# Performance work log

Hardware: AMD Instinct MI355X
Metric: run time of the kernel (lower is better)

## Reference

```python
import jax, jax.numpy as jnp
import numpy as np

N_NODES = 300000   # cell instances
N_NETS  = 200000   # hyperedges (nets); each net has exactly one source/driver
E_SINK  = 1000000  # sink (node->net) pin edges
NODE_DIM, NET_DIM, EMB = 32, 16, 64
L, NUM_VN = 3, 1000
OUT_NODE, OUT_NET = 4, 4
SLOPE = 0.01  # torch leaky_relu default negative_slope


def leaky(x):
    return jnp.where(x >= 0, x, SLOPE * x)


def _lin(key, fan_in, fan_out):
    kw, kb = jax.random.split(key)
    b = 1.0 / np.sqrt(fan_in)
    W = jax.random.uniform(kw, (fan_in, fan_out), jnp.float32, -b, b)
    bb = jax.random.uniform(kb, (fan_out,), jnp.float32, -b, b)
    return W, bb


def setup_inputs() -> dict:
    key = jax.random.key(0)
    ks = iter(jax.random.split(key, 64))
    d = {}
    d["node_features"] = jax.random.normal(next(ks), (N_NODES, NODE_DIM), jnp.float32)
    d["net_features"] = jax.random.normal(next(ks), (N_NETS, NET_DIM), jnp.float32)
    d["src_nodes"] = jax.random.randint(next(ks), (N_NETS,), 0, N_NODES)   # driver node of net i
    d["sink_nodes"] = jax.random.randint(next(ks), (E_SINK,), 0, N_NODES)
    d["sink_nets"] = jax.random.randint(next(ks), (E_SINK,), 0, N_NETS)
    d["edge_weight"] = jax.random.uniform(next(ks), (E_SINK,), jnp.float32)
    d["batch"] = jax.random.randint(next(ks), (N_NODES,), 0, NUM_VN)       # node -> virtual node id
    # node / net encoders
    d["ne_W1"], d["ne_b1"] = _lin(next(ks), NODE_DIM, 2 * EMB)
    d["ne_W2"], d["ne_b2"] = _lin(next(ks), 2 * EMB, EMB)
    d["te_W1"], d["te_b1"] = _lin(next(ks), NET_DIM, EMB)
    d["te_W2"], d["te_b2"] = _lin(next(ks), EMB, EMB)
    d["vn_emb"] = jnp.zeros((EMB,), jnp.float32)  # torch: init.constant_(weight, 0)
    # HyperConv layers, stacked over L
    Wnet, bnet, Wnode, bnode = [], [], [], []
    for _ in range(L):
        W, b = _lin(next(ks), 3 * EMB, EMB); Wnet.append(W); bnet.append(b)
        W, b = _lin(next(ks), 2 * EMB, EMB); Wnode.append(W); bnode.append(b)
    d["conv_Wnet"] = jnp.stack(Wnet); d["conv_bnet"] = jnp.stack(bnet)
    d["conv_Wnode"] = jnp.stack(Wnode); d["conv_bnode"] = jnp.stack(bnode)
    # virtual-node MLPs (L-1 of them)
    vW1, vb1, vW2, vb2 = [], [], [], []
    for _ in range(L - 1):
        W, b = _lin(next(ks), EMB, EMB); vW1.append(W); vb1.append(b)
        W, b = _lin(next(ks), EMB, EMB); vW2.append(W); vb2.append(b)
    d["vn_W1"] = jnp.stack(vW1); d["vn_b1"] = jnp.stack(vb1)
    d["vn_W2"] = jnp.stack(vW2); d["vn_b2"] = jnp.stack(vb2)
    # output heads
    d["fc1n_W"], d["fc1n_b"] = _lin(next(ks), EMB, 256)
    d["fc2n_W"], d["fc2n_b"] = _lin(next(ks), 256, OUT_NODE)
    d["fc1e_W"], d["fc1e_b"] = _lin(next(ks), EMB, 64)
    d["fc2e_W"], d["fc2e_b"] = _lin(next(ks), 64, OUT_NET)
    return d


def _forward(node_features, net_features, edge_weight,
             ne_W1, ne_b1, ne_W2, ne_b2, te_W1, te_b1, te_W2, te_b2,
             vn_emb, conv_Wnet, conv_bnet, conv_Wnode, conv_bnode,
             vn_W1, vn_b1, vn_W2, vn_b2,
             fc1n_W, fc1n_b, fc2n_W, fc2n_b, fc1e_W, fc1e_b, fc2e_W, fc2e_b,
             src_nodes, sink_nodes, sink_nets, batch):
    h = leaky(node_features @ ne_W1 + ne_b1) @ ne_W2 + ne_b2   # [N, EMB]
    g = leaky(net_features @ te_W1 + te_b1) @ te_W2 + te_b2    # [M, EMB]
    w = edge_weight[:, None]
    vn = jnp.broadcast_to(vn_emb, (NUM_VN, EMB))               # embedding of all-zero indices
    for l in range(L):
        h = h + vn[batch]
        # node -> net (hyperedge) aggregation: driver message + weighted sink sum
        agg_src = h[src_nodes]                                             # [M, EMB]
        agg_sink = jax.ops.segment_sum(h[sink_nodes] * w, sink_nets, num_segments=N_NETS)
        g = jnp.concatenate([g, agg_src, agg_sink], axis=-1) @ conv_Wnet[l] + conv_bnet[l]
        # net -> node aggregation
        back = jax.ops.segment_sum(g, src_nodes, num_segments=N_NODES) \
             + jax.ops.segment_sum(g[sink_nets] * w, sink_nodes, num_segments=N_NODES)
        h = jnp.concatenate([h, back], axis=-1) @ conv_Wnode[l] + conv_bnode[l]
        h = leaky(h)
        g = leaky(g)
        if l < L - 1:
            pooled = jax.ops.segment_max(h, batch, num_segments=NUM_VN)   # global_max_pool
            tmp = pooled + vn
            vn = vn + (leaky(tmp @ vn_W1[l] + vn_b1[l]) @ vn_W2[l] + vn_b2[l])
    node_rep = jnp.abs(leaky(h @ fc1n_W + fc1n_b) @ fc2n_W + fc2n_b)
    net_rep = jnp.abs(leaky(g @ fc1e_W + fc1e_b) @ fc2e_W + fc2e_b)
    return node_rep, net_rep


def reference(node_features, net_features, edge_weight,
              ne_W1, ne_b1, ne_W2, ne_b2, te_W1, te_b1, te_W2, te_b2,
              vn_emb, conv_Wnet, conv_bnet, conv_Wnode, conv_bnode,
              vn_W1, vn_b1, vn_W2, vn_b2,
              fc1n_W, fc1n_b, fc2n_W, fc2n_b, fc1e_W, fc1e_b, fc2e_W, fc2e_b,
              src_nodes, sink_nodes, sink_nets, batch):
    return _forward(node_features, net_features, edge_weight,
                    ne_W1, ne_b1, ne_W2, ne_b2, te_W1, te_b1, te_W2, te_b2,
                    vn_emb, conv_Wnet, conv_bnet, conv_Wnode, conv_bnode,
                    vn_W1, vn_b1, vn_W2, vn_b2,
                    fc1n_W, fc1n_b, fc2n_W, fc2n_b, fc1e_W, fc1e_b, fc2e_W, fc2e_b,
                    src_nodes, sink_nodes, sink_nets, batch)
```

## Files before the change

kernel.cpp:

```cpp
#include <hip/hip_runtime.h>
#include <cstdint>

static constexpr int N_NODES = 300000;
static constexpr int N_NETS  = 200000;
static constexpr int E_SINK  = 1000000;
static constexpr int NODE_DIM = 32;
static constexpr int NET_DIM  = 16;
static constexpr int EMB = 64;
static constexpr int NUM_VN = 1000;
#define SLOPE 0.01f

typedef __attribute__((ext_vector_type(8))) short bhalf8;
typedef __attribute__((ext_vector_type(4))) float floatx4;
typedef unsigned short u16;

__device__ __forceinline__ float leaky(float x) { return x >= 0.f ? x : SLOPE * x; }

__device__ __forceinline__ unsigned bf16_rne(float x) {
    unsigned u = __float_as_uint(x);
    return (u + 0x7FFFu + ((u >> 16) & 1u)) >> 16;
}
__device__ __forceinline__ void split1(float x, u16& hh, u16& ll) {
    unsigned hb = bf16_rne(x);
    float fh = __uint_as_float(hb << 16);
    unsigned lb = bf16_rne(x - fh);
    hh = (u16)hb; ll = (u16)lb;
}
__device__ __forceinline__ void split8v(const float* x, bhalf8& ah, bhalf8& al) {
#pragma unroll
    for (int e = 0; e < 8; ++e) {
        u16 hh, ll; split1(x[e], hh, ll);
        ah[e] = (short)hh; al[e] = (short)ll;
    }
}
__device__ __forceinline__ float rec1(short h, short l) {
    return __uint_as_float(((unsigned)(u16)h) << 16) +
           __uint_as_float(((unsigned)(u16)l) << 16);
}

__device__ __forceinline__ void afrag_f32(const float* rowp, int kbase, bhalf8& ah, bhalf8& al) {
    float4 v0 = *(const float4*)(rowp + kbase);
    float4 v1 = *(const float4*)(rowp + kbase + 4);
    float x[8] = {v0.x, v0.y, v0.z, v0.w, v1.x, v1.y, v1.z, v1.w};
    split8v(x, ah, al);
}
__device__ __forceinline__ void afrag_hl(const u16* hi, const u16* lo, size_t off,
                                         bhalf8& ah, bhalf8& al) {
    ah = *(const bhalf8*)(hi + off);
    al = *(const bhalf8*)(lo + off);
}

__device__ __forceinline__ floatx4 mm3(bhalf8 ah, bhalf8 al, bhalf8 wh, bhalf8 wl, floatx4 c) {
    c = __builtin_amdgcn_mfma_f32_16x16x32_bf16(ah, wh, c, 0, 0, 0);
    c = __builtin_amdgcn_mfma_f32_16x16x32_bf16(ah, wl, c, 0, 0, 0);
    c = __builtin_amdgcn_mfma_f32_16x16x32_bf16(al, wh, c, 0, 0, 0);
    return c;
}

static constexpr int OFF_NEW1 = 0;
static constexpr int OFF_NEW2 = 4096;
static constexpr int OFF_TEW1 = 12288;
static constexpr int OFF_TEW2 = 14336;
static constexpr int OFF_CWNET = 18432;
static constexpr int OFF_CWNODE = 55296;
static constexpr int OFF_FC1N = 79872;
static constexpr int OFF_FC1E = 96256;
static constexpr int W_TOTAL  = 100352;

__global__ void k_prep_w(const float* __restrict__ neW1, const float* __restrict__ neW2,
                         const float* __restrict__ teW1, const float* __restrict__ teW2,
                         const float* __restrict__ cWnet, const float* __restrict__ cWnode,
                         const float* __restrict__ fc1n, const float* __restrict__ fc1e,
                         u16* __restrict__ wfh, u16* __restrict__ wfl)
{
    int i = blockIdx.x * 256 + threadIdx.x;
    if (i >= W_TOTAL) return;
    int r, ncols, K; const float* src;
    if (i < OFF_NEW2)        { r = i;             src = neW1;  ncols = 128; K = 32; }
    else if (i < OFF_TEW1)   { r = i - OFF_NEW2;  src = neW2;  ncols = 64;  K = 128; }
    else if (i < OFF_TEW2)   { r = i - OFF_TEW1;  src = teW1;  ncols = 64;  K = 16; }
    else if (i < OFF_CWNET)  { r = i - OFF_TEW2;  src = teW2;  ncols = 64;  K = 64; }
    else if (i < OFF_CWNODE) { int t = i - OFF_CWNET;  int l = t / 12288; r = t % 12288;
                               src = cWnet + (size_t)l * 192 * 64; ncols = 64; K = 192; }
    else if (i < OFF_FC1N)   { int t = i - OFF_CWNODE; int l = t / 8192;  r = t % 8192;
                               src = cWnode + (size_t)l * 128 * 64; ncols = 64; K = 128; }
    else if (i < OFF_FC1E)   { r = i - OFF_FC1N;  src = fc1n;  ncols = 256; K = 64; }
    else                     { r = i - OFF_FC1E;  src = fc1e;  ncols = 64;  K = 64; }
    int e = r & 7, g = (r >> 3) & 3;
    int cidx = r >> 5;
    int col = cidx % ncols, kt = cidx / ncols;
    int k = kt * 32 + g * 8 + e;
    float v = (k < K) ? src[(size_t)k * ncols + col] : 0.f;
    u16 hh, ll; split1(v, hh, ll);
    wfh[i] = hh; wfl[i] = ll;
}

__device__ __forceinline__ bhalf8 ldw(const u16* p, int idx) {
    return *(const bhalf8*)(p + idx);
}

__global__ void k_hist_edges(const int* __restrict__ sink_nets, const int* __restrict__ sink_nodes,
                             int* __restrict__ cnt_net, int* __restrict__ cnt_node)
{
    int e = blockIdx.x * 256 + threadIdx.x;
    if (e >= E_SINK) return;
    atomicAdd(&cnt_net[sink_nets[e]], 1);
    atomicAdd(&cnt_node[sink_nodes[e]], 1);
}

__global__ void k_hist_misc(const int* __restrict__ src_nodes, const int* __restrict__ batch,
                            int* __restrict__ cnt_src, int* __restrict__ cnt_vn)
{
    int i = blockIdx.x * 256 + threadIdx.x;
    if (i < N_NETS) atomicAdd(&cnt_src[src_nodes[i]], 1);
    if (i < N_NODES) atomicAdd(&cnt_vn[batch[i]], 1);
}

__global__ void k_scan1(const int* __restrict__ cnt, int n, int* __restrict__ bsum) {
    __shared__ int s[256];
    int i = blockIdx.x * 256 + threadIdx.x;
    s[threadIdx.x] = (i < n) ? cnt[i] : 0;
    __syncthreads();
    for (int off = 128; off; off >>= 1) {
        if (threadIdx.x < off) s[threadIdx.x] += s[threadIdx.x + off];
        __syncthreads();
    }
    if (threadIdx.x == 0) bsum[blockIdx.x] = s[0];
}

__global__ void k_scan2(int* __restrict__ data, int n) {
    __shared__ int s[256];
    __shared__ int carry_s;
    int tid = threadIdx.x;
    if (tid == 0) carry_s = 0;
    __syncthreads();
    for (int base = 0; base < n; base += 256) {
        int i = base + tid;
        int v = (i < n) ? data[i] : 0;
        s[tid] = v;
        __syncthreads();
        for (int off = 1; off < 256; off <<= 1) {
            int t = (tid >= off) ? s[tid - off] : 0;
            __syncthreads();
            s[tid] += t;
            __syncthreads();
        }
        int excl = s[tid] - v + carry_s;
        if (i < n) data[i] = excl;
        __syncthreads();
        if (tid == 255) carry_s = excl + v;
        __syncthreads();
    }
}

__global__ void k_scan3(const int* __restrict__ cnt, int n, const int* __restrict__ bsum,
                        int* __restrict__ start) {
    __shared__ int s[256];
    int i = blockIdx.x * 256 + threadIdx.x;
    int v = (i < n) ? cnt[i] : 0;
    s[threadIdx.x] = v;
    __syncthreads();
    for (int off = 1; off < 256; off <<= 1) {
        int t = (threadIdx.x >= off) ? s[threadIdx.x - off] : 0;
        __syncthreads();
        s[threadIdx.x] += t;
        __syncthreads();
    }
    int excl = s[threadIdx.x] - v + bsum[blockIdx.x];
    if (i < n) start[i] = excl;
    if (i == n - 1) start[n] = excl + v;
}

__global__ void k_fill_edges(const int* __restrict__ sink_nets, const int* __restrict__ sink_nodes,
                             const float* __restrict__ ew,
                             const int* __restrict__ net_start, const int* __restrict__ node_start,
                             int* __restrict__ cur_net, int* __restrict__ cur_node,
                             int2* __restrict__ e_pack, int2* __restrict__ e2_pack)
{
    int e = blockIdx.x * 256 + threadIdx.x;
    if (e >= E_SINK) return;
    int tn = sink_nets[e], dn = sink_nodes[e];
    int wbits = __float_as_int(ew[e]);
    int p = net_start[tn] + atomicAdd(&cur_net[tn], 1);
    e_pack[p] = make_int2(dn, wbits);
    int q = node_start[dn] + atomicAdd(&cur_node[dn], 1);
    e2_pack[q] = make_int2(tn, wbits);
}

__global__ void k_fill_misc(const int* __restrict__ src_nodes, const int* __restrict__ batch,
                            const int* __restrict__ src_start, const int* __restrict__ vn_start,
                            int* __restrict__ cur_src, int* __restrict__ cur_vn,
                            int* __restrict__ s_net, int* __restrict__ b_node)
{
    int i = blockIdx.x * 256 + threadIdx.x;
    if (i < N_NETS) {
        int d = src_nodes[i];
        int p = src_start[d] + atomicAdd(&cur_src[d], 1);
        s_net[p] = i;
    }
    if (i < N_NODES) {
        int v = batch[i];
        int p = vn_start[v] + atomicAdd(&cur_vn[v], 1);
        b_node[p] = i;
    }
}

template<bool HF32>
__global__ __launch_bounds__(256) void k_gather_agg(
    u16* __restrict__ agg_hi, u16* __restrict__ agg_lo,
    const u16* __restrict__ h_hi, const u16* __restrict__ h_lo, const float* __restrict__ h_f32,
    const int* __restrict__ net_start, const int2* __restrict__ e_pack)
{
    int w = (blockIdx.x * 256 + threadIdx.x) >> 6;
    if (w >= N_NETS) return;
    int lane = threadIdx.x & 63;
    int grp = lane >> 3, l8 = lane & 7;
    int j0 = net_start[w], j1 = net_start[w + 1];
    float a[8] = {0.f, 0.f, 0.f, 0.f, 0.f, 0.f, 0.f, 0.f};
    for (int j = j0 + grp; j < j1; j += 8) {
        int2 pk = e_pack[j];
        float wt = __int_as_float(pk.y);
        if (HF32) {
            const float4* rp = (const float4*)(h_f32 + (size_t)pk.x * 64 + l8 * 8);
            float4 v0 = rp[0], v1 = rp[1];
            a[0] += wt * v0.x; a[1] += wt * v0.y; a[2] += wt * v0.z; a[3] += wt * v0.w;
            a[4] += wt * v1.x; a[5] += wt * v1.y; a[6] += wt * v1.z; a[7] += wt * v1.w;
        } else {
            size_t off = (size_t)pk.x * 64 + l8 * 8;
            bhalf8 vh = *(const bhalf8*)(h_hi + off);
            bhalf8 vl = *(const bhalf8*)(h_lo + off);
#pragma unroll
            for (int e = 0; e < 8; ++e) a[e] += wt * rec1(vh[e], vl[e]);
        }
    }
#pragma unroll
    for (int e = 0; e < 8; ++e) {
        a[e] += __shfl_xor(a[e], 8, 64);
        a[e] += __shfl_xor(a[e], 16, 64);
        a[e] += __shfl_xor(a[e], 32, 64);
    }
    if (grp == 0) {
        bhalf8 oh, ol;
        split8v(a, oh, ol);
        size_t off = (size_t)w * 64 + l8 * 8;
        *(bhalf8*)(agg_hi + off) = oh;
        *(bhalf8*)(agg_lo + off) = ol;
    }
}

template<bool GF32>
__global__ __launch_bounds__(256) void k_gather_back(
    u16* __restrict__ back_hi, u16* __restrict__ back_lo,
    const u16* __restrict__ g_hi, const u16* __restrict__ g_lo, const float* __restrict__ g_raw,
    const int* __restrict__ src_start, const int* __restrict__ s_net,
    const int* __restrict__ node_start, const int2* __restrict__ e2_pack)
{
    int w = (blockIdx.x * 256 + threadIdx.x) >> 6;
    if (w >= N_NODES) return;
    int lane = threadIdx.x & 63;
    int grp = lane >> 3, l8 = lane & 7;
    float a[8] = {0.f, 0.f, 0.f, 0.f, 0.f, 0.f, 0.f, 0.f};
    int j0 = src_start[w], j1 = src_start[w + 1];
    for (int j = j0 + grp; j < j1; j += 8) {
        int idx = s_net[j];
        if (GF32) {
            const float4* rp = (const float4*)(g_raw + (size_t)idx * 64 + l8 * 8);
            float4 v0 = rp[0], v1 = rp[1];
            a[0] += v0.x; a[1] += v0.y; a[2] += v0.z; a[3] += v0.w;
            a[4] += v1.x; a[5] += v1.y; a[6] += v1.z; a[7] += v1.w;
        } else {
            size_t off = (size_t)idx * 64 + l8 * 8;
            bhalf8 vh = *(const bhalf8*)(g_hi + off);
            bhalf8 vl = *(const bhalf8*)(g_lo + off);
#pragma unroll
            for (int e = 0; e < 8; ++e) {
                float f = rec1(vh[e], vl[e]);
                a[e] += (f >= 0.f) ? f : f * 100.f;
            }
        }
    }
    j0 = node_start[w]; j1 = node_start[w + 1];
    for (int j = j0 + grp; j < j1; j += 8) {
        int2 pk = e2_pack[j];
        float wt = __int_as_float(pk.y);
        if (GF32) {
            const float4* rp = (const float4*)(g_raw + (size_t)pk.x * 64 + l8 * 8);
            float4 v0 = rp[0], v1 = rp[1];
            a[0] += wt * v0.x; a[1] += wt * v0.y; a[2] += wt * v0.z; a[3] += wt * v0.w;
            a[4] += wt * v1.x; a[5] += wt * v1.y; a[6] += wt * v1.z; a[7] += wt * v1.w;
        } else {
            size_t off = (size_t)pk.x * 64 + l8 * 8;
            bhalf8 vh = *(const bhalf8*)(g_hi + off);
            bhalf8 vl = *(const bhalf8*)(g_lo + off);
#pragma unroll
            for (int e = 0; e < 8; ++e) {
                float f = rec1(vh[e], vl[e]);
                a[e] += wt * ((f >= 0.f) ? f : f * 100.f);
            }
        }
    }
#pragma unroll
    for (int e = 0; e < 8; ++e) {
        a[e] += __shfl_xor(a[e], 8, 64);
        a[e] += __shfl_xor(a[e], 16, 64);
        a[e] += __shfl_xor(a[e], 32, 64);
    }
    if (grp == 0) {
        bhalf8 oh, ol;
        split8v(a, oh, ol);
        size_t off = (size_t)w * 64 + l8 * 8;
        *(bhalf8*)(back_hi + off) = oh;
        *(bhalf8*)(back_lo + off) = ol;
    }
}

template<bool HF32>
__global__ __launch_bounds__(256) void k_pool_gather(
    float* __restrict__ pooled, const u16* __restrict__ h_hi, const u16* __restrict__ h_lo,
    const float* __restrict__ h_f32,
    const int* __restrict__ vn_start, const int* __restrict__ b_node)
{
    __shared__ float red[32][64];
    int tid = threadIdx.x;
    int grp = tid >> 3, l8 = tid & 7;
    int v = blockIdx.x;
    int j0 = vn_start[v], j1 = vn_start[v + 1];
    const float NEG = -__builtin_inff();
    float m[8] = {NEG, NEG, NEG, NEG, NEG, NEG, NEG, NEG};
    for (int j = j0 + grp; j < j1; j += 32) {
        int nd = b_node[j];
        if (HF32) {
            const float4* rp = (const float4*)(h_f32 + (size_t)nd * 64 + l8 * 8);
            float4 v0 = rp[0], v1 = rp[1];
            m[0] = fmaxf(m[0], v0.x); m[1] = fmaxf(m[1], v0.y);
            m[2] = fmaxf(m[2], v0.z); m[3] = fmaxf(m[3], v0.w);
            m[4] = fmaxf(m[4], v1.x); m[5] = fmaxf(m[5], v1.y);
            m[6] = fmaxf(m[6], v1.z); m[7] = fmaxf(m[7], v1.w);
        } else {
            size_t off = (size_t)nd * 64 + l8 * 8;
            bhalf8 vh = *(const bhalf8*)(h_hi + off);
            bhalf8 vl = *(const bhalf8*)(h_lo + off);
#pragma unroll
            for (int e = 0; e < 8; ++e) m[e] = fmaxf(m[e], rec1(vh[e], vl[e]));
        }
    }
#pragma unroll
    for (int e = 0; e < 8; ++e) red[grp][l8 * 8 + e] = m[e];
    __syncthreads();
    if (tid < 64) {
        float mm = red[0][tid];
#pragma unroll
        for (int q = 1; q < 32; ++q) mm = fmaxf(mm, red[q][tid]);
        pooled[(size_t)v * 64 + tid] = mm;
    }
}

__global__ __launch_bounds__(256) void k_node_enc(
    const float* __restrict__ x, const u16* __restrict__ wfh, const u16* __restrict__ wfl,
    const float* __restrict__ b1, const float* __restrict__ b2,
    u16* __restrict__ h_hi, u16* __restrict__ h_lo, float* __restrict__ h_f32)
{
    __shared__ u16 t_hi[64][136];
    __shared__ u16 t_lo[64][136];
    int lane = threadIdx.x & 63, wid = threadIdx.x >> 6;
    int g16 = lane >> 4, l15 = lane & 15;
    int rbase = blockIdx.x * 64;

    bhalf8 W1H[2], W1L[2];
#pragma unroll
    for (int s = 0; s < 2; ++s) {
        int col = wid * 16 + s * 64 + l15;
        int fo = OFF_NEW1 + (col * 4 + g16) * 8;
        W1H[s] = ldw(wfh, fo); W1L[s] = ldw(wfl, fo);
    }
    bhalf8 W2H[4], W2L[4];
    int cs = wid * 16 + l15;
#pragma unroll
    for (int kt = 0; kt < 4; ++kt) {
        int fo = OFF_NEW2 + ((kt * 64 + cs) * 4 + g16) * 8;
        W2H[kt] = ldw(wfh, fo); W2L[kt] = ldw(wfl, fo);
    }

#pragma unroll
    for (int ms = 0; ms < 4; ++ms) {
        int r = min(rbase + ms * 16 + l15, N_NODES - 1);
        bhalf8 ah, al;
        afrag_f32(x + (size_t)r * NODE_DIM, g16 * 8, ah, al);
#pragma unroll
        for (int s = 0; s < 2; ++s) {
            floatx4 acc = {0.f, 0.f, 0.f, 0.f};
            acc = mm3(ah, al, W1H[s], W1L[s], acc);
            int hc = wid * 16 + s * 64 + l15;
            float bb = b1[hc];
#pragma unroll
            for (int i = 0; i < 4; ++i) {
                u16 hh, ll;
                split1(leaky(acc[i] + bb), hh, ll);
                t_hi[ms * 16 + g16 * 4 + i][hc] = hh;
                t_lo[ms * 16 + g16 * 4 + i][hc] = ll;
            }
        }
    }
    __syncthreads();

    float bias = b2[cs];
#pragma unroll
    for (int ms = 0; ms < 4; ++ms) {
        floatx4 acc = {0.f, 0.f, 0.f, 0.f};
#pragma unroll
        for (int kt = 0; kt < 4; ++kt) {
            bhalf8 ah = *(const bhalf8*)(&t_hi[ms * 16 + l15][kt * 32 + g16 * 8]);
            bhalf8 al = *(const bhalf8*)(&t_lo[ms * 16 + l15][kt * 32 + g16 * 8]);
            acc = mm3(ah, al, W2H[kt], W2L[kt], acc);
        }
#pragma unroll
        for (int i = 0; i < 4; ++i) {
            int r = rbase + ms * 16 + g16 * 4 + i;
            if (r < N_NODES) {
                float v = acc[i] + bias;
                if (h_f32) h_f32[(size_t)r * 64 + cs] = v;
                u16 hh, ll;
                split1(v, hh, ll);
                h_hi[(size_t)r * 64 + cs] = hh;
                h_lo[(size_t)r * 64 + cs] = ll;
            }
        }
    }
}

__global__ __launch_bounds__(256) void k_net_enc(
    const float* __restrict__ x, const u16* __restrict__ wfh, const u16* __restrict__ wfl,
    const float* __restrict__ b1, const float* __restrict__ b2,
    u16* __restrict__ g_hi, u16* __restrict__ g_lo)
{
    __shared__ u16 t_hi[64][72];
    __shared__ u16 t_lo[64][72];
    int lane = threadIdx.x & 63, wid = threadIdx.x >> 6;
    int g16 = lane >> 4, l15 = lane & 15;
    int rbase = blockIdx.x * 64;
    int cs = wid * 16 + l15;

    int fo = OFF_TEW1 + (cs * 4 + g16) * 8;
    bhalf8 W1H = ldw(wfh, fo), W1L = ldw(wfl, fo);
    bhalf8 W2H[2], W2L[2];
#pragma unroll
    for (int kt = 0; kt < 2; ++kt) {
        int f2 = OFF_TEW2 + ((kt * 64 + cs) * 4 + g16) * 8;
        W2H[kt] = ldw(wfh, f2); W2L[kt] = ldw(wfl, f2);
    }

#pragma unroll
    for (int ms = 0; ms < 4; ++ms) {
        int r = min(rbase + ms * 16 + l15, N_NETS - 1);
        bhalf8 ah = {0,0,0,0,0,0,0,0}, al = {0,0,0,0,0,0,0,0};
        if (g16 < 2) afrag_f32(x + (size_t)r * NET_DIM, g16 * 8, ah, al);
        floatx4 acc = {0.f, 0.f, 0.f, 0.f};
        acc = mm3(ah, al, W1H, W1L, acc);
        float bb = b1[cs];
#pragma unroll
        for (int i = 0; i < 4; ++i) {
            u16 hh, ll;
            split1(leaky(acc[i] + bb), hh, ll);
            t_hi[ms * 16 + g16 * 4 + i][cs] = hh;
            t_lo[ms * 16 + g16 * 4 + i][cs] = ll;
        }
    }
    __syncthreads();

    float bias = b2[cs];
#pragma unroll
    for (int ms = 0; ms < 4; ++ms) {
        floatx4 acc = {0.f, 0.f, 0.f, 0.f};
#pragma unroll
        for (int kt = 0; kt < 2; ++kt) {
            bhalf8 ah = *(const bhalf8*)(&t_hi[ms * 16 + l15][kt * 32 + g16 * 8]);
            bhalf8 al = *(const bhalf8*)(&t_lo[ms * 16 + l15][kt * 32 + g16 * 8]);
            acc = mm3(ah, al, W2H[kt], W2L[kt], acc);
        }
#pragma unroll
        for (int i = 0; i < 4; ++i) {
            int r = rbase + ms * 16 + g16 * 4 + i;
            if (r < N_NETS) {
                u16 hh, ll;
                split1(acc[i] + bias, hh, ll);
                g_hi[(size_t)r * 64 + cs] = hh;
                g_lo[(size_t)r * 64 + cs] = ll;
            }
        }
    }
}

__global__ void k_vn_init(float* __restrict__ vn, const float* __restrict__ vn_emb) {
    int idx = blockIdx.x * blockDim.x + threadIdx.x;
    if (idx < NUM_VN * EMB) vn[idx] = vn_emb[idx & 63];
}

__global__ void k_add_vn(u16* __restrict__ h_hi, u16* __restrict__ h_lo, float* __restrict__ h_f32,
                         const float* __restrict__ vn, const int* __restrict__ batch) {
    int idx = blockIdx.x * blockDim.x + threadIdx.x;
    if (idx >= N_NODES * 8) return;
    int n = idx >> 3, c8 = idx & 7;
    size_t off = (size_t)n * 64 + c8 * 8;
    const float* vr = vn + (size_t)batch[n] * 64 + c8 * 8;
    float out[8];
    if (h_f32) {
        const float4* hp = (const float4*)(h_f32 + off);
        float4 v0 = hp[0], v1 = hp[1];
        out[0] = v0.x + vr[0]; out[1] = v0.y + vr[1]; out[2] = v0.z + vr[2]; out[3] = v0.w + vr[3];
        out[4] = v1.x + vr[4]; out[5] = v1.y + vr[5]; out[6] = v1.z + vr[6]; out[7] = v1.w + vr[7];
        float4* wp = (float4*)(h_f32 + off);
        wp[0] = make_float4(out[0], out[1], out[2], out[3]);
        wp[1] = make_float4(out[4], out[5], out[6], out[7]);
    } else {
        bhalf8 vh = *(const bhalf8*)(h_hi + off);
        bhalf8 vl = *(const bhalf8*)(h_lo + off);
#pragma unroll
        for (int e = 0; e < 8; ++e) out[e] = rec1(vh[e], vl[e]) + vr[e];
    }
    bhalf8 oh, ol;
    split8v(out, oh, ol);
    *(bhalf8*)(h_hi + off) = oh;
    *(bhalf8*)(h_lo + off) = ol;
}

__global__ __launch_bounds__(256) void k_conv_net(
    u16* g_hi, u16* g_lo, float* __restrict__ g_raw,
    const u16* __restrict__ h_hi, const u16* __restrict__ h_lo,
    const u16* __restrict__ s_hi, const u16* __restrict__ s_lo,
    const int* __restrict__ src,
    const u16* __restrict__ wfh, const u16* __restrict__ wfl, int wbase,
    const float* __restrict__ b)
{
    int lane = threadIdx.x & 63, wid = threadIdx.x >> 6;
    int g16 = lane >> 4, l15 = lane & 15;
    int rbase = blockIdx.x * 64;
    int cs = wid * 16 + l15;

    bhalf8 WH[6], WL[6];
#pragma unroll
    for (int kt = 0; kt < 6; ++kt) {
        int fo = wbase + ((kt * 64 + cs) * 4 + g16) * 8;
        WH[kt] = ldw(wfh, fo); WL[kt] = ldw(wfl, fo);
    }

    bhalf8 GH[4][2], GL[4][2];
#pragma unroll
    for (int ms = 0; ms < 4; ++ms) {
        int r = min(rbase + ms * 16 + l15, N_NETS - 1);
#pragma unroll
        for (int kt = 0; kt < 2; ++kt)
            afrag_hl(g_hi, g_lo, (size_t)r * 64 + kt * 32 + g16 * 8, GH[ms][kt], GL[ms][kt]);
    }
    __syncthreads();

    float bias = b[cs];
#pragma unroll
    for (int ms = 0; ms < 4; ++ms) {
        floatx4 acc = {0.f, 0.f, 0.f, 0.f};
#pragma unroll
        for (int kt = 0; kt < 2; ++kt) acc = mm3(GH[ms][kt], GL[ms][kt], WH[kt], WL[kt], acc);
        int ar = min(rbase + ms * 16 + l15, N_NETS - 1);
        size_t srow = (size_t)src[ar] * 64;
#pragma unroll
        for (int kt = 0; kt < 2; ++kt) {
            bhalf8 ah, al;
            afrag_hl(h_hi, h_lo, srow + kt * 32 + g16 * 8, ah, al);
            acc = mm3(ah, al, WH[2 + kt], WL[2 + kt], acc);
        }
#pragma unroll
        for (int kt = 0; kt < 2; ++kt) {
            bhalf8 ah, al;
            afrag_hl(s_hi, s_lo, (size_t)ar * 64 + kt * 32 + g16 * 8, ah, al);
            acc = mm3(ah, al, WH[4 + kt], WL[4 + kt], acc);
        }
#pragma unroll
        for (int i = 0; i < 4; ++i) {
            int r = rbase + ms * 16 + g16 * 4 + i;
            if (r < N_NETS) {
                float graw = acc[i] + bias;
                if (g_raw) g_raw[(size_t)r * 64 + cs] = graw;
                u16 hh, ll;
                split1(leaky(graw), hh, ll);
                g_hi[(size_t)r * 64 + cs] = hh;
                g_lo[(size_t)r * 64 + cs] = ll;
            }
        }
    }
}

__global__ __launch_bounds__(256) void k_conv_node(
    u16* h_hi, u16* h_lo, float* __restrict__ h_f32,
    const u16* __restrict__ s_hi, const u16* __restrict__ s_lo,
    const u16* __restrict__ wfh, const u16* __restrict__ wfl, int wbase,
    const float* __restrict__ b)
{
    int lane = threadIdx.x & 63, wid = threadIdx.x >> 6;
    int g16 = lane >> 4, l15 = lane & 15;
    int rbase = blockIdx.x * 64;
    int cs = wid * 16 + l15;

    bhalf8 WH[4], WL[4];
#pragma unroll
    for (int kt = 0; kt < 4; ++kt) {
        int fo = wbase + ((kt * 64 + cs) * 4 + g16) * 8;
        WH[kt] = ldw(wfh, fo); WL[kt] = ldw(wfl, fo);
    }

    bhalf8 HH[4][2], HL[4][2];
#pragma unroll
    for (int ms = 0; ms < 4; ++ms) {
        int r = min(rbase + ms * 16 + l15, N_NODES - 1);
#pragma unroll
        for (int kt = 0; kt < 2; ++kt)
            afrag_hl(h_hi, h_lo, (size_t)r * 64 + kt * 32 + g16 * 8, HH[ms][kt], HL[ms][kt]);
    }
    __syncthreads();

    float bias = b[cs];
#pragma unroll
    for (int ms = 0; ms < 4; ++ms) {
        floatx4 acc = {0.f, 0.f, 0.f, 0.f};
#pragma unroll
        for (int kt = 0; kt < 2; ++kt) acc = mm3(HH[ms][kt], HL[ms][kt], WH[kt], WL[kt], acc);
        int ar = min(rbase + ms * 16 + l15, N_NODES - 1);
#pragma unroll
        for (int kt = 0; kt < 2; ++kt) {
            bhalf8 ah, al;
            afrag_hl(s_hi, s_lo, (size_t)ar * 64 + kt * 32 + g16 * 8, ah, al);
            acc = mm3(ah, al, WH[2 + kt], WL[2 + kt], acc);
        }
#pragma unroll
        for (int i = 0; i < 4; ++i) {
            int r = rbase + ms * 16 + g16 * 4 + i;
            if (r < N_NODES) {
                float hval = leaky(acc[i] + bias);
                if (h_f32) h_f32[(size_t)r * 64 + cs] = hval;
                u16 hh, ll;
                split1(hval, hh, ll);
                h_hi[(size_t)r * 64 + cs] = hh;
                h_lo[(size_t)r * 64 + cs] = ll;
            }
        }
    }
}

__global__ __launch_bounds__(256) void k_vn_update(
    float* __restrict__ vn, const float* __restrict__ pooled,
    const float* __restrict__ W1, const float* __restrict__ b1,
    const float* __restrict__ W2, const float* __restrict__ b2)
{
    int wv = threadIdx.x >> 6, lane = threadIdx.x & 63;
    int v = blockIdx.x * 4 + wv;
    if (v >= NUM_VN) return;
    float p = pooled[(size_t)v * 64 + lane];
    float vv = vn[v * 64 + lane];
    float tmp = p + vv;
    float t1 = b1[lane];
#pragma unroll 16
    for (int k = 0; k < 64; ++k) t1 += __shfl(tmp, k, 64) * W1[k * 64 + lane];
    t1 = leaky(t1);
    float t2 = b2[lane];
#pragma unroll 16
    for (int k = 0; k < 64; ++k) t2 += __shfl(t1, k, 64) * W2[k * 64 + lane];
    vn[v * 64 + lane] = vv + t2;
}

__global__ __launch_bounds__(256) void k_fc_node(
    float* __restrict__ out, const u16* __restrict__ h_hi, const u16* __restrict__ h_lo,
    const u16* __restrict__ wfh, const u16* __restrict__ wfl,
    const float* __restrict__ b1, const float* __restrict__ W2, const float* __restrict__ b2)
{
    __shared__ float red[4][64][4];
    int lane = threadIdx.x & 63, wid = threadIdx.x >> 6;
    int g16 = lane >> 4, l15 = lane & 15;
    int rbase = blockIdx.x * 64;

    bhalf8 W1H[4][2], W1L[4][2];
    float4 w2v[4];
    float b1v[4];
#pragma unroll
    for (int s = 0; s < 4; ++s) {
        int hc = wid * 16 + s * 64 + l15;
#pragma unroll
        for (int kt = 0; kt < 2; ++kt) {
            int fo = OFF_FC1N + ((kt * 256 + hc) * 4 + g16) * 8;
            W1H[s][kt] = ldw(wfh, fo); W1L[s][kt] = ldw(wfl, fo);
        }
        w2v[s] = *(const float4*)(W2 + hc * 4);
        b1v[s] = b1[hc];
    }

#pragma unroll
    for (int ms = 0; ms < 4; ++ms) {
        int r = min(rbase + ms * 16 + l15, N_NODES - 1);
        bhalf8 ah[2], al[2];
#pragma unroll
        for (int kt = 0; kt < 2; ++kt)
            afrag_hl(h_hi, h_lo, (size_t)r * 64 + kt * 32 + g16 * 8, ah[kt], al[kt]);
        float po[4][4] = {{0.f,0.f,0.f,0.f},{0.f,0.f,0.f,0.f},{0.f,0.f,0.f,0.f},{0.f,0.f,0.f,0.f}};
#pragma unroll
        for (int s = 0; s < 4; ++s) {
            floatx4 acc = {0.f, 0.f, 0.f, 0.f};
#pragma unroll
            for (int kt = 0; kt < 2; ++kt) acc = mm3(ah[kt], al[kt], W1H[s][kt], W1L[s][kt], acc);
#pragma unroll
            for (int i = 0; i < 4; ++i) {
                float act = leaky(acc[i] + b1v[s]);
                po[i][0] += act * w2v[s].x;
                po[i][1] += act * w2v[s].y;
                po[i][2] += act * w2v[s].z;
                po[i][3] += act * w2v[s].w;
            }
        }
#pragma unroll
        for (int i = 0; i < 4; ++i)
#pragma unroll
            for (int o = 0; o < 4; ++o) {
                po[i][o] += __shfl_xor(po[i][o], 1, 64);
                po[i][o] += __shfl_xor(po[i][o], 2, 64);
                po[i][o] += __shfl_xor(po[i][o], 4, 64);
                po[i][o] += __shfl_xor(po[i][o], 8, 64);
            }
        if (l15 == 0) {
#pragma unroll
            for (int i = 0; i < 4; ++i)
#pragma unroll
                for (int o = 0; o < 4; ++o)
                    red[wid][ms * 16 + g16 * 4 + i][o] = po[i][o];
        }
    }
    __syncthreads();
    int tid = threadIdx.x;
    int row = tid >> 2, o = tid & 3;
    float sum = red[0][row][o] + red[1][row][o] + red[2][row][o] + red[3][row][o];
    int r = rbase + row;
    if (r < N_NODES) out[(size_t)r * 4 + o] = fabsf(sum + b2[o]);
}

__global__ __launch_bounds__(256) void k_fc_net(
    float* __restrict__ out, const u16* __restrict__ g_hi, const u16* __restrict__ g_lo,
    const u16* __restrict__ wfh, const u16* __restrict__ wfl,
    const float* __restrict__ b1, const float* __restrict__ W2, const float* __restrict__ b2)
{
    __shared__ float red[4][64][4];
    int lane = threadIdx.x & 63, wid = threadIdx.x >> 6;
    int g16 = lane >> 4, l15 = lane & 15;
    int rbase = blockIdx.x * 64;
    int cs = wid * 16 + l15;

    bhalf8 W1H[2], W1L[2];
#pragma unroll
    for (int kt = 0; kt < 2; ++kt) {
        int fo = OFF_FC1E + ((kt * 64 + cs) * 4 + g16) * 8;
        W1H[kt] = ldw(wfh, fo); W1L[kt] = ldw(wfl, fo);
    }
    float4 w2v = *(const float4*)(W2 + cs * 4);
    float b1v = b1[cs];

#pragma unroll
    for (int ms = 0; ms < 4; ++ms) {
        int r = min(rbase + ms * 16 + l15, N_NETS - 1);
        bhalf8 ah[2], al[2];
#pragma unroll
        for (int kt = 0; kt < 2; ++kt)
            afrag_hl(g_hi, g_lo, (size_t)r * 64 + kt * 32 + g16 * 8, ah[kt], al[kt]);
        floatx4 acc = {0.f, 0.f, 0.f, 0.f};
#pragma unroll
        for (int kt = 0; kt < 2; ++kt) acc = mm3(ah[kt], al[kt], W1H[kt], W1L[kt], acc);
        float po[4][4];
#pragma unroll
        for (int i = 0; i < 4; ++i) {
            float act = leaky(acc[i] + b1v);
            po[i][0] = act * w2v.x;
            po[i][1] = act * w2v.y;
            po[i][2] = act * w2v.z;
            po[i][3] = act * w2v.w;
        }
#pragma unroll
        for (int i = 0; i < 4; ++i)
#pragma unroll
            for (int o = 0; o < 4; ++o) {
                po[i][o] += __shfl_xor(po[i][o], 1, 64);
                po[i][o] += __shfl_xor(po[i][o], 2, 64);
                po[i][o] += __shfl_xor(po[i][o], 4, 64);
                po[i][o] += __shfl_xor(po[i][o], 8, 64);
            }
        if (l15 == 0) {
#pragma unroll
            for (int i = 0; i < 4; ++i)
#pragma unroll
                for (int o = 0; o < 4; ++o)
                    red[wid][ms * 16 + g16 * 4 + i][o] = po[i][o];
        }
    }
    __syncthreads();
    int tid = threadIdx.x;
    int row = tid >> 2, o = tid & 3;
    float sum = red[0][row][o] + red[1][row][o] + red[2][row][o] + red[3][row][o];
    int r = rbase + row;
    if (r < N_NETS) out[(size_t)r * 4 + o] = fabsf(sum + b2[o]);
}

extern "C" void kernel_launch(void* const* d_in, const int* in_sizes, int n_in,
                              void* d_out, int out_size, void* d_ws, size_t ws_size,
                              hipStream_t stream)
{
    const float* node_features = (const float*)d_in[0];
    const float* net_features  = (const float*)d_in[1];
    const int*   src_nodes     = (const int*)d_in[2];
    const int*   sink_nodes    = (const int*)d_in[3];
    const int*   sink_nets     = (const int*)d_in[4];
    const float* edge_weight   = (const float*)d_in[5];
    const int*   batch         = (const int*)d_in[6];
    const float* ne_W1 = (const float*)d_in[7];
    const float* ne_b1 = (const float*)d_in[8];
    const float* ne_W2 = (const float*)d_in[9];
    const float* ne_b2 = (const float*)d_in[10];
    const float* te_W1 = (const float*)d_in[11];
    const float* te_b1 = (const float*)d_in[12];
    const float* te_W2 = (const float*)d_in[13];
    const float* te_b2 = (const float*)d_in[14];
    const float* vn_emb = (const float*)d_in[15];
    const float* conv_Wnet  = (const float*)d_in[16];
    const float* conv_bnet  = (const float*)d_in[17];
    const float* conv_Wnode = (const float*)d_in[18];
    const float* conv_bnode = (const float*)d_in[19];
    const float* vn_W1 = (const float*)d_in[20];
    const float* vn_b1 = (const float*)d_in[21];
    const float* vn_W2 = (const float*)d_in[22];
    const float* vn_b2 = (const float*)d_in[23];
    const float* fc1n_W = (const float*)d_in[24];
    const float* fc1n_b = (const float*)d_in[25];
    const float* fc2n_W = (const float*)d_in[26];
    const float* fc2n_b = (const float*)d_in[27];
    const float* fc1e_W = (const float*)d_in[28];
    const float* fc1e_b = (const float*)d_in[29];
    const float* fc2e_W = (const float*)d_in[30];
    const float* fc2e_b = (const float*)d_in[31];

    float* out_node = (float*)d_out;
    float* out_net  = out_node + (size_t)N_NODES * 4;

    char* wsp = (char*)d_ws;
    size_t used = 0;
    auto alloc = [&](size_t bytes) -> char* {
        char* r = wsp + used;
        used += (bytes + 255) & ~(size_t)255;
        return r;
    };
    u16* h_hi = (u16*)alloc((size_t)N_NODES * 64 * 2);
    u16* h_lo = (u16*)alloc((size_t)N_NODES * 64 * 2);
    u16* g_hi = (u16*)alloc((size_t)N_NETS * 64 * 2);
    u16* g_lo = (u16*)alloc((size_t)N_NETS * 64 * 2);
    u16* s_hi = (u16*)alloc((size_t)N_NODES * 64 * 2);
    u16* s_lo = (u16*)alloc((size_t)N_NODES * 64 * 2);
    u16* wfh  = (u16*)alloc((size_t)W_TOTAL * 2);
    u16* wfl  = (u16*)alloc((size_t)W_TOTAL * 2);
    float* vn     = (float*)alloc((size_t)NUM_VN * EMB * 4);
    float* pooled = (float*)alloc((size_t)NUM_VN * EMB * 4);
    int* net_start  = (int*)alloc((size_t)(N_NETS + 1) * 4);
    int* node_start = (int*)alloc((size_t)(N_NODES + 1) * 4);
    int* src_start  = (int*)alloc((size_t)(N_NODES + 1) * 4);
    int* vn_start   = (int*)alloc((size_t)(NUM_VN + 1) * 4);
    int2* e_pack  = (int2*)alloc((size_t)E_SINK * 8);
    int2* e2_pack = (int2*)alloc((size_t)E_SINK * 8);
    int* s_net  = (int*)alloc((size_t)N_NETS * 4);
    int* b_node = (int*)alloc((size_t)N_NODES * 4);
    const int CNT_TOTAL = N_NETS + N_NODES + N_NODES + NUM_VN;
    int* cnt  = (int*)alloc((size_t)CNT_TOTAL * 4);
    int* bsum = (int*)alloc(2048 * 4);
    int* cnt_net  = cnt;
    int* cnt_node = cnt + N_NETS;
    int* cnt_src  = cnt_node + N_NODES;
    int* cnt_vn   = cnt_src + N_NODES;

    float* g_raw = nullptr;
    if (used + (size_t)N_NETS * 64 * 4 + 256 <= ws_size)
        g_raw = (float*)alloc((size_t)N_NETS * 64 * 4);
    float* h_f32 = nullptr;
    if (used + (size_t)N_NODES * 64 * 4 + 256 <= ws_size)
        h_f32 = (float*)alloc((size_t)N_NODES * 64 * 4);

    const int nodeTiles = (N_NODES + 63) / 64;
    const int netTiles  = (N_NETS + 63) / 64;
    const int vnBlocks  = (NUM_VN + 3) / 4;
    const int vnElemBlocks  = (NUM_VN * EMB + 255) / 256;
    const int addVnBlocks  = (N_NODES * 8 + 255) / 256;
    const int edgeThreadBlocks = (E_SINK + 255) / 256;
    const int miscThreadBlocks = (N_NODES + 255) / 256;
    const int netWaveBlocks  = (N_NETS + 3) / 4;
    const int nodeWaveBlocks = (N_NODES + 3) / 4;
    const int prepBlocks = (W_TOTAL + 255) / 256;

    hipMemsetAsync(cnt, 0, (size_t)CNT_TOTAL * sizeof(int), stream);
    k_hist_edges<<<edgeThreadBlocks, 256, 0, stream>>>(sink_nets, sink_nodes, cnt_net, cnt_node);
    k_hist_misc<<<miscThreadBlocks, 256, 0, stream>>>(src_nodes, batch, cnt_src, cnt_vn);

    auto scan = [&](int* cnt_arr, int n, int* start_arr) {
        int nb = (n + 255) / 256;
        k_scan1<<<nb, 256, 0, stream>>>(cnt_arr, n, bsum);
        k_scan2<<<1, 256, 0, stream>>>(bsum, nb);
        k_scan3<<<nb, 256, 0, stream>>>(cnt_arr, n, bsum, start_arr);
    };
    scan(cnt_net, N_NETS, net_start);
    scan(cnt_node, N_NODES, node_start);
    scan(cnt_src, N_NODES, src_start);
    scan(cnt_vn, NUM_VN, vn_start);

    hipMemsetAsync(cnt, 0, (size_t)CNT_TOTAL * sizeof(int), stream);
    k_fill_edges<<<edgeThreadBlocks, 256, 0, stream>>>(sink_nets, sink_nodes, edge_weight,
        net_start, node_start, cnt_net, cnt_node, e_pack, e2_pack);
    k_fill_misc<<<miscThreadBlocks, 256, 0, stream>>>(src_nodes, batch, src_start, vn_start,
        cnt_src, cnt_vn, s_net, b_node);

    k_prep_w<<<prepBlocks, 256, 0, stream>>>(ne_W1, ne_W2, te_W1, te_W2,
                                             conv_Wnet, conv_Wnode, fc1n_W, fc1e_W, wfh, wfl);
    k_node_enc<<<nodeTiles, 256, 0, stream>>>(node_features, wfh, wfl, ne_b1, ne_b2,
                                              h_hi, h_lo, h_f32);
    k_net_enc<<<netTiles, 256, 0, stream>>>(net_features, wfh, wfl, te_b1, te_b2, g_hi, g_lo);
    k_vn_init<<<vnElemBlocks, 256, 0, stream>>>(vn, vn_emb);

    for (int l = 0; l < 3; ++l) {
        k_add_vn<<<addVnBlocks, 256, 0, stream>>>(h_hi, h_lo, h_f32, vn, batch);

        if (h_f32)
            k_gather_agg<true><<<netWaveBlocks, 256, 0, stream>>>(s_hi, s_lo, h_hi, h_lo, h_f32,
                                                                  net_start, e_pack);
        else
            k_gather_agg<false><<<netWaveBlocks, 256, 0, stream>>>(s_hi, s_lo, h_hi, h_lo, h_f32,
                                                                   net_start, e_pack);

        k_conv_net<<<netTiles, 256, 0, stream>>>(g_hi, g_lo, g_raw, h_hi, h_lo, s_hi, s_lo,
            src_nodes, wfh, wfl, OFF_CWNET + l * 12288, conv_bnet + (size_t)l * 64);

        if (g_raw)
            k_gather_back<true><<<nodeWaveBlocks, 256, 0, stream>>>(s_hi, s_lo, g_hi, g_lo, g_raw,
                src_start, s_net, node_start, e2_pack);
        else
            k_gather_back<false><<<nodeWaveBlocks, 256, 0, stream>>>(s_hi, s_lo, g_hi, g_lo, g_raw,
                src_start, s_net, node_start, e2_pack);

        k_conv_node<<<nodeTiles, 256, 0, stream>>>(h_hi, h_lo, h_f32, s_hi, s_lo,
            wfh, wfl, OFF_CWNODE + l * 8192, conv_bnode + (size_t)l * 64);

        if (l < 2) {
            if (h_f32)
                k_pool_gather<true><<<NUM_VN, 256, 0, stream>>>(pooled, h_hi, h_lo, h_f32,
                                                                vn_start, b_node);
            else
                k_pool_gather<false><<<NUM_VN, 256, 0, stream>>>(pooled, h_hi, h_lo, h_f32,
                                                                 vn_start, b_node);
            k_vn_update<<<vnBlocks, 256, 0, stream>>>(vn, pooled,
                vn_W1 + (size_t)l * 64 * 64, vn_b1 + (size_t)l * 64,
                vn_W2 + (size_t)l * 64 * 64, vn_b2 + (size_t)l * 64);
        }
    }

    k_fc_node<<<nodeTiles, 256, 0, stream>>>(out_node, h_hi, h_lo, wfh, wfl,
                                             fc1n_b, fc2n_W, fc2n_b);
    k_fc_net<<<netTiles, 256, 0, stream>>>(out_net, g_hi, g_lo, wfh, wfl,
                                           fc1e_b, fc2e_W, fc2e_b);
}
```

Before: 1.779 ms.

## Store activations as single fp32 buffers and split to bf16 hi/lo at MFMA load

Node, net and aggregate activations are now kept as plain fp32 arrays instead of paired bf16 hi/lo arrays plus optional fp32 copies. The hi/lo split now happens when the MFMA kernels load their fragments, using a cheaper truncating split. The net stores raw pre-activation values with leaky applied on read (lk0 flag), which removes the inverse-leaky reconstruction in gather_back. This cuts duplicate writes and the dual-path storage but adds split ALU work in the GEMM kernels and changes rounding from RNE to truncation.

```diff
diff --git a/kernel.cpp b/kernel.cpp
--- a/kernel.cpp
+++ b/kernel.cpp
@@ -26,28 +26,32 @@
     unsigned lb = bf16_rne(x - fh);
     hh = (u16)hb; ll = (u16)lb;
 }
-__device__ __forceinline__ void split8v(const float* x, bhalf8& ah, bhalf8& al) {
+
+__device__ __forceinline__ void csplit8(const float* x, bhalf8& ah, bhalf8& al) {
 #pragma unroll
     for (int e = 0; e < 8; ++e) {
-        u16 hh, ll; split1(x[e], hh, ll);
-        ah[e] = (short)hh; al[e] = (short)ll;
-    }
-}
-__device__ __forceinline__ float rec1(short h, short l) {
-    return __uint_as_float(((unsigned)(u16)h) << 16) +
-           __uint_as_float(((unsigned)(u16)l) << 16);
-}
-
-__device__ __forceinline__ void afrag_f32(const float* rowp, int kbase, bhalf8& ah, bhalf8& al) {
+        unsigned u = __float_as_uint(x[e]);
+        ah[e] = (short)(u >> 16);
+        float d = x[e] - __uint_as_float(u & 0xFFFF0000u);
+        al[e] = (short)(__float_as_uint(d) >> 16);
+    }
+}
+template<bool LK>
+__device__ __forceinline__ void afrag32(const float* rowp, int kbase, bhalf8& ah, bhalf8& al) {
     float4 v0 = *(const float4*)(rowp + kbase);
     float4 v1 = *(const float4*)(rowp + kbase + 4);
     float x[8] = {v0.x, v0.y, v0.z, v0.w, v1.x, v1.y, v1.z, v1.w};
-    split8v(x, ah, al);
-}
-__device__ __forceinline__ void afrag_hl(const u16* hi, const u16* lo, size_t off,
-                                         bhalf8& ah, bhalf8& al) {
-    ah = *(const bhalf8*)(hi + off);
-    al = *(const bhalf8*)(lo + off);
+    if (LK) {
+#pragma unroll
+        for (int e = 0; e < 8; ++e) x[e] = leaky(x[e]);
+    }
+    csplit8(x, ah, al);
+}
+__device__ __forceinline__ void afragl(const float* tp, bhalf8& ah, bhalf8& al) {
+    float4 v0 = *(const float4*)tp;
+    float4 v1 = *(const float4*)(tp + 4);
+    float x[8] = {v0.x, v0.y, v0.z, v0.w, v1.x, v1.y, v1.z, v1.w};
+    csplit8(x, ah, al);
 }
 
 __device__ __forceinline__ floatx4 mm3(bhalf8 ah, bhalf8 al, bhalf8 wh, bhalf8 wl, floatx4 c) {
@@ -205,10 +209,8 @@
     }
 }
 
-template<bool HF32>
 __global__ __launch_bounds__(256) void k_gather_agg(
-    u16* __restrict__ agg_hi, u16* __restrict__ agg_lo,
-    const u16* __restrict__ h_hi, const u16* __restrict__ h_lo, const float* __restrict__ h_f32,
+    float* __restrict__ agg, const float* __restrict__ h,
     const int* __restrict__ net_start, const int2* __restrict__ e_pack)
 {
     int w = (blockIdx.x * 256 + threadIdx.x) >> 6;
@@ -220,18 +222,10 @@
     for (int j = j0 + grp; j < j1; j += 8) {
         int2 pk = e_pack[j];
         float wt = __int_as_float(pk.y);
-        if (HF32) {
-            const float4* rp = (const float4*)(h_f32 + (size_t)pk.x * 64 + l8 * 8);
-            float4 v0 = rp[0], v1 = rp[1];
-            a[0] += wt * v0.x; a[1] += wt * v0.y; a[2] += wt * v0.z; a[3] += wt * v0.w;
-            a[4] += wt * v1.x; a[5] += wt * v1.y; a[6] += wt * v1.z; a[7] += wt * v1.w;
-        } else {
-            size_t off = (size_t)pk.x * 64 + l8 * 8;
-            bhalf8 vh = *(const bhalf8*)(h_hi + off);
-            bhalf8 vl = *(const bhalf8*)(h_lo + off);
-#pragma unroll
-            for (int e = 0; e < 8; ++e) a[e] += wt * rec1(vh[e], vl[e]);
-        }
+        const float4* rp = (const float4*)(h + (size_t)pk.x * 64 + l8 * 8);
+        float4 v0 = rp[0], v1 = rp[1];
+        a[0] += wt * v0.x; a[1] += wt * v0.y; a[2] += wt * v0.z; a[3] += wt * v0.w;
+        a[4] += wt * v1.x; a[5] += wt * v1.y; a[6] += wt * v1.z; a[7] += wt * v1.w;
     }
 #pragma unroll
     for (int e = 0; e < 8; ++e) {
@@ -240,18 +234,14 @@
         a[e] += __shfl_xor(a[e], 32, 64);
     }
     if (grp == 0) {
-        bhalf8 oh, ol;
-        split8v(a, oh, ol);
-        size_t off = (size_t)w * 64 + l8 * 8;
-        *(bhalf8*)(agg_hi + off) = oh;
-        *(bhalf8*)(agg_lo + off) = ol;
-    }
-}
-
-template<bool GF32>
+        float4* op = (float4*)(agg + (size_t)w * 64 + l8 * 8);
+        op[0] = make_float4(a[0], a[1], a[2], a[3]);
+        op[1] = make_float4(a[4], a[5], a[6], a[7]);
+    }
+}
+
 __global__ __launch_bounds__(256) void k_gather_back(
-    u16* __restrict__ back_hi, u16* __restrict__ back_lo,
-    const u16* __restrict__ g_hi, const u16* __restrict__ g_lo, const float* __restrict__ g_raw,
+    float* __restrict__ back, const float* __restrict__ g,
     const int* __restrict__ src_start, const int* __restrict__ s_net,
     const int* __restrict__ node_start, const int2* __restrict__ e2_pack)
 {
@@ -263,41 +253,19 @@
     int j0 = src_start[w], j1 = src_start[w + 1];
     for (int j = j0 + grp; j < j1; j += 8) {
         int idx = s_net[j];
-        if (GF32) {
-            const float4* rp = (const float4*)(g_raw + (size_t)idx * 64 + l8 * 8);
-            float4 v0 = rp[0], v1 = rp[1];
-            a[0] += v0.x; a[1] += v0.y; a[2] += v0.z; a[3] += v0.w;
-            a[4] += v1.x; a[5] += v1.y; a[6] += v1.z; a[7] += v1.w;
-        } else {
-            size_t off = (size_t)idx * 64 + l8 * 8;
-            bhalf8 vh = *(const bhalf8*)(g_hi + off);
-            bhalf8 vl = *(const bhalf8*)(g_lo + off);
-#pragma unroll
-            for (int e = 0; e < 8; ++e) {
-                float f = rec1(vh[e], vl[e]);
-                a[e] += (f >= 0.f) ? f : f * 100.f;
-            }
-        }
+        const float4* rp = (const float4*)(g + (size_t)idx * 64 + l8 * 8);
+        float4 v0 = rp[0], v1 = rp[1];
+        a[0] += v0.x; a[1] += v0.y; a[2] += v0.z; a[3] += v0.w;
+        a[4] += v1.x; a[5] += v1.y; a[6] += v1.z; a[7] += v1.w;
     }
     j0 = node_start[w]; j1 = node_start[w + 1];
     for (int j = j0 + grp; j < j1; j += 8) {
         int2 pk = e2_pack[j];
         float wt = __int_as_float(pk.y);
-        if (GF32) {
-            const float4* rp = (const float4*)(g_raw + (size_t)pk.x * 64 + l8 * 8);
-            float4 v0 = rp[0], v1 = rp[1];
-            a[0] += wt * v0.x; a[1] += wt * v0.y; a[2] += wt * v0.z; a[3] += wt * v0.w;
-            a[4] += wt * v1.x; a[5] += wt * v1.y; a[6] += wt * v1.z; a[7] += wt * v1.w;
-        } else {
-            size_t off = (size_t)pk.x * 64 + l8 * 8;
-            bhalf8 vh = *(const bhalf8*)(g_hi + off);
-            bhalf8 vl = *(const bhalf8*)(g_lo + off);
-#pragma unroll
-            for (int e = 0; e < 8; ++e) {
-                float f = rec1(vh[e], vl[e]);
-                a[e] += wt * ((f >= 0.f) ? f : f * 100.f);
-            }
-        }
+        const float4* rp = (const float4*)(g + (size_t)pk.x * 64 + l8 * 8);
+        float4 v0 = rp[0], v1 = rp[1];
+        a[0] += wt * v0.x; a[1] += wt * v0.y; a[2] += wt * v0.z; a[3] += wt * v0.w;
+        a[4] += wt * v1.x; a[5] += wt * v1.y; a[6] += wt * v1.z; a[7] += wt * v1.w;
     }
 #pragma unroll
     for (int e = 0; e < 8; ++e) {
@@ -306,18 +274,14 @@
         a[e] += __shfl_xor(a[e], 32, 64);
     }
     if (grp == 0) {
-        bhalf8 oh, ol;
-        split8v(a, oh, ol);
-        size_t off = (size_t)w * 64 + l8 * 8;
-        *(bhalf8*)(back_hi + off) = oh;
-        *(bhalf8*)(back_lo + off) = ol;
-    }
-}
-
-template<bool HF32>
+        float4* op = (float4*)(back + (size_t)w * 64 + l8 * 8);
+        op[0] = make_float4(a[0], a[1], a[2], a[3]);
+        op[1] = make_float4(a[4], a[5], a[6], a[7]);
+    }
+}
+
 __global__ __launch_bounds__(256) void k_pool_gather(
-    float* __restrict__ pooled, const u16* __restrict__ h_hi, const u16* __restrict__ h_lo,
-    const float* __restrict__ h_f32,
+    float* __restrict__ pooled, const float* __restrict__ h,
     const int* __restrict__ vn_start, const int* __restrict__ b_node)
 {
     __shared__ float red[32][64];
@@ -329,20 +293,12 @@
     float m[8] = {NEG, NEG, NEG, NEG, NEG, NEG, NEG, NEG};
     for (int j = j0 + grp; j < j1; j += 32) {
         int nd = b_node[j];
-        if (HF32) {
-            const float4* rp = (const float4*)(h_f32 + (size_t)nd * 64 + l8 * 8);
-            float4 v0 = rp[0], v1 = rp[1];
-            m[0] = fmaxf(m[0], v0.x); m[1] = fmaxf(m[1], v0.y);
-            m[2] = fmaxf(m[2], v0.z); m[3] = fmaxf(m[3], v0.w);
-            m[4] = fmaxf(m[4], v1.x); m[5] = fmaxf(m[5], v1.y);
-            m[6] = fmaxf(m[6], v1.z); m[7] = fmaxf(m[7], v1.w);
-        } else {
-            size_t off = (size_t)nd * 64 + l8 * 8;
-            bhalf8 vh = *(const bhalf8*)(h_hi + off);
-            bhalf8 vl = *(const bhalf8*)(h_lo + off);
-#pragma unroll
-            for (int e = 0; e < 8; ++e) m[e] = fmaxf(m[e], rec1(vh[e], vl[e]));
-        }
+        const float4* rp = (const float4*)(h + (size_t)nd * 64 + l8 * 8);
+        float4 v0 = rp[0], v1 = rp[1];
+        m[0] = fmaxf(m[0], v0.x); m[1] = fmaxf(m[1], v0.y);
+        m[2] = fmaxf(m[2], v0.z); m[3] = fmaxf(m[3], v0.w);
+        m[4] = fmaxf(m[4], v1.x); m[5] = fmaxf(m[5], v1.y);
+        m[6] = fmaxf(m[6], v1.z); m[7] = fmaxf(m[7], v1.w);
     }
 #pragma unroll
     for (int e = 0; e < 8; ++e) red[grp][l8 * 8 + e] = m[e];
@@ -357,14 +313,13 @@
 
 __global__ __launch_bounds__(256) void k_node_enc(
     const float* __restrict__ x, const u16* __restrict__ wfh, const u16* __restrict__ wfl,
-    const float* __restrict__ b1, const float* __restrict__ b2,
-    u16* __restrict__ h_hi, u16* __restrict__ h_lo, float* __restrict__ h_f32)
-{
-    __shared__ u16 t_hi[64][136];
-    __shared__ u16 t_lo[64][136];
+    const float* __restrict__ b1, const float* __restrict__ b2, float* __restrict__ h)
+{
+    __shared__ __align__(16) float t[64][132];
     int lane = threadIdx.x & 63, wid = threadIdx.x >> 6;
     int g16 = lane >> 4, l15 = lane & 15;
     int rbase = blockIdx.x * 64;
+    int cs = wid * 16 + l15;
 
     bhalf8 W1H[2], W1L[2];
 #pragma unroll
@@ -374,7 +329,6 @@
         W1H[s] = ldw(wfh, fo); W1L[s] = ldw(wfl, fo);
     }
     bhalf8 W2H[4], W2L[4];
-    int cs = wid * 16 + l15;
 #pragma unroll
     for (int kt = 0; kt < 4; ++kt) {
         int fo = OFF_NEW2 + ((kt * 64 + cs) * 4 + g16) * 8;
@@ -385,7 +339,7 @@
     for (int ms = 0; ms < 4; ++ms) {
         int r = min(rbase + ms * 16 + l15, N_NODES - 1);
         bhalf8 ah, al;
-        afrag_f32(x + (size_t)r * NODE_DIM, g16 * 8, ah, al);
+        afrag32<false>(x + (size_t)r * NODE_DIM, g16 * 8, ah, al);
 #pragma unroll
         for (int s = 0; s < 2; ++s) {
             floatx4 acc = {0.f, 0.f, 0.f, 0.f};
@@ -393,12 +347,8 @@
             int hc = wid * 16 + s * 64 + l15;
             float bb = b1[hc];
 #pragma unroll
-            for (int i = 0; i < 4; ++i) {
-                u16 hh, ll;
-                split1(leaky(acc[i] + bb), hh, ll);
-                t_hi[ms * 16 + g16 * 4 + i][hc] = hh;
-                t_lo[ms * 16 + g16 * 4 + i][hc] = ll;
-            }
+            for (int i = 0; i < 4; ++i)
+                t[ms * 16 + g16 * 4 + i][hc] = leaky(acc[i] + bb);
         }
     }
     __syncthreads();
@@ -409,32 +359,23 @@
         floatx4 acc = {0.f, 0.f, 0.f, 0.f};
 #pragma unroll
         for (int kt = 0; kt < 4; ++kt) {
-            bhalf8 ah = *(const bhalf8*)(&t_hi[ms * 16 + l15][kt * 32 + g16 * 8]);
-            bhalf8 al = *(const bhalf8*)(&t_lo[ms * 16 + l15][kt * 32 + g16 * 8]);
+            bhalf8 ah, al;
+            afragl(&t[ms * 16 + l15][kt * 32 + g16 * 8], ah, al);
             acc = mm3(ah, al, W2H[kt], W2L[kt], acc);
         }
 #pragma unroll
         for (int i = 0; i < 4; ++i) {
             int r = rbase + ms * 16 + g16 * 4 + i;
-            if (r < N_NODES) {
-                float v = acc[i] + bias;
-                if (h_f32) h_f32[(size_t)r * 64 + cs] = v;
-                u16 hh, ll;
-                split1(v, hh, ll);
-                h_hi[(size_t)r * 64 + cs] = hh;
-                h_lo[(size_t)r * 64 + cs] = ll;
-            }
+            if (r < N_NODES) h[(size_t)r * 64 + cs] = acc[i] + bias;
         }
     }
 }
 
 __global__ __launch_bounds__(256) void k_net_enc(
     const float* __restrict__ x, const u16* __restrict__ wfh, const u16* __restrict__ wfl,
-    const float* __restrict__ b1, const float* __restrict__ b2,
-    u16* __restrict__ g_hi, u16* __restrict__ g_lo)
-{
-    __shared__ u16 t_hi[64][72];
-    __shared__ u16 t_lo[64][72];
+    const float* __restrict__ b1, const float* __restrict__ b2, float* __restrict__ g)
+{
+    __shared__ __align__(16) float t[64][68];
     int lane = threadIdx.x & 63, wid = threadIdx.x >> 6;
     int g16 = lane >> 4, l15 = lane & 15;
     int rbase = blockIdx.x * 64;
@@ -453,17 +394,13 @@
     for (int ms = 0; ms < 4; ++ms) {
         int r = min(rbase + ms * 16 + l15, N_NETS - 1);
         bhalf8 ah = {0,0,0,0,0,0,0,0}, al = {0,0,0,0,0,0,0,0};
-        if (g16 < 2) afrag_f32(x + (size_t)r * NET_DIM, g16 * 8, ah, al);
+        if (g16 < 2) afrag32<false>(x + (size_t)r * NET_DIM, g16 * 8, ah, al);
         floatx4 acc = {0.f, 0.f, 0.f, 0.f};
         acc = mm3(ah, al, W1H, W1L, acc);
         float bb = b1[cs];
 #pragma unroll
-        for (int i = 0; i < 4; ++i) {
-            u16 hh, ll;
-            split1(leaky(acc[i] + bb), hh, ll);
-            t_hi[ms * 16 + g16 * 4 + i][cs] = hh;
-            t_lo[ms * 16 + g16 * 4 + i][cs] = ll;
-        }
+        for (int i = 0; i < 4; ++i)
+            t[ms * 16 + g16 * 4 + i][cs] = leaky(acc[i] + bb);
     }
     __syncthreads();
 
@@ -473,19 +410,14 @@
         floatx4 acc = {0.f, 0.f, 0.f, 0.f};
 #pragma unroll
         for (int kt = 0; kt < 2; ++kt) {
-            bhalf8 ah = *(const bhalf8*)(&t_hi[ms * 16 + l15][kt * 32 + g16 * 8]);
-            bhalf8 al = *(const bhalf8*)(&t_lo[ms * 16 + l15][kt * 32 + g16 * 8]);
+            bhalf8 ah, al;
+            afragl(&t[ms * 16 + l15][kt * 32 + g16 * 8], ah, al);
             acc = mm3(ah, al, W2H[kt], W2L[kt], acc);
         }
 #pragma unroll
         for (int i = 0; i < 4; ++i) {
             int r = rbase + ms * 16 + g16 * 4 + i;
-            if (r < N_NETS) {
-                u16 hh, ll;
-                split1(acc[i] + bias, hh, ll);
-                g_hi[(size_t)r * 64 + cs] = hh;
-                g_lo[(size_t)r * 64 + cs] = ll;
-            }
+            if (r < N_NETS) g[(size_t)r * 64 + cs] = acc[i] + bias;
         }
     }
 }
@@ -495,41 +427,21 @@
     if (idx < NUM_VN * EMB) vn[idx] = vn_emb[idx & 63];
 }
 
-__global__ void k_add_vn(u16* __restrict__ h_hi, u16* __restrict__ h_lo, float* __restrict__ h_f32,
-                         const float* __restrict__ vn, const int* __restrict__ batch) {
+__global__ void k_add_vn(float4* __restrict__ h4, const float* __restrict__ vn,
+                         const int* __restrict__ batch) {
     int idx = blockIdx.x * blockDim.x + threadIdx.x;
-    if (idx >= N_NODES * 8) return;
-    int n = idx >> 3, c8 = idx & 7;
-    size_t off = (size_t)n * 64 + c8 * 8;
-    const float* vr = vn + (size_t)batch[n] * 64 + c8 * 8;
-    float out[8];
-    if (h_f32) {
-        const float4* hp = (const float4*)(h_f32 + off);
-        float4 v0 = hp[0], v1 = hp[1];
-        out[0] = v0.x + vr[0]; out[1] = v0.y + vr[1]; out[2] = v0.z + vr[2]; out[3] = v0.w + vr[3];
-        out[4] = v1.x + vr[4]; out[5] = v1.y + vr[5]; out[6] = v1.z + vr[6]; out[7] = v1.w + vr[7];
-        float4* wp = (float4*)(h_f32 + off);
-        wp[0] = make_float4(out[0], out[1], out[2], out[3]);
-        wp[1] = make_float4(out[4], out[5], out[6], out[7]);
-    } else {
-        bhalf8 vh = *(const bhalf8*)(h_hi + off);
-        bhalf8 vl = *(const bhalf8*)(h_lo + off);
-#pragma unroll
-        for (int e = 0; e < 8; ++e) out[e] = rec1(vh[e], vl[e]) + vr[e];
-    }
-    bhalf8 oh, ol;
-    split8v(out, oh, ol);
-    *(bhalf8*)(h_hi + off) = oh;
-    *(bhalf8*)(h_lo + off) = ol;
+    if (idx >= N_NODES * 16) return;
+    int n = idx >> 4, c4 = idx & 15;
+    const float4* vr = (const float4*)(vn + (size_t)batch[n] * 64);
+    float4 hv = h4[idx], vv = vr[c4];
+    h4[idx] = make_float4(hv.x + vv.x, hv.y + vv.y, hv.z + vv.z, hv.w + vv.w);
 }
 
 __global__ __launch_bounds__(256) void k_conv_net(
-    u16* g_hi, u16* g_lo, float* __restrict__ g_raw,
-    const u16* __restrict__ h_hi, const u16* __restrict__ h_lo,
-    const u16* __restrict__ s_hi, const u16* __restrict__ s_lo,
+    float* __restrict__ g, const float* __restrict__ h, const float* __restrict__ s,
     const int* __restrict__ src,
     const u16* __restrict__ wfh, const u16* __restrict__ wfl, int wbase,
-    const float* __restrict__ b)
+    const float* __restrict__ b, int lk0)
 {
     int lane = threadIdx.x & 63, wid = threadIdx.x >> 6;
     int g16 = lane >> 4, l15 = lane & 15;
@@ -547,9 +459,12 @@
 #pragma unroll
     for (int ms = 0; ms < 4; ++ms) {
         int r = min(rbase + ms * 16 + l15, N_NETS - 1);
-#pragma unroll
-        for (int kt = 0; kt < 2; ++kt)
-            afrag_hl(g_hi, g_lo, (size_t)r * 64 + kt * 32 + g16 * 8, GH[ms][kt], GL[ms][kt]);
+        const float* rp = g + (size_t)r * 64;
+#pragma unroll
+        for (int kt = 0; kt < 2; ++kt) {
+            if (lk0) afrag32<true>(rp, kt * 32 + g16 * 8, GH[ms][kt], GL[ms][kt]);
+            else     afrag32<false>(rp, kt * 32 + g16 * 8, GH[ms][kt], GL[ms][kt]);
+        }
     }
     __syncthreads();
 
@@ -560,37 +475,30 @@
 #pragma unroll
         for (int kt = 0; kt < 2; ++kt) acc = mm3(GH[ms][kt], GL[ms][kt], WH[kt], WL[kt], acc);
         int ar = min(rbase + ms * 16 + l15, N_NETS - 1);
-        size_t srow = (size_t)src[ar] * 64;
+        const float* hp = h + (size_t)src[ar] * 64;
 #pragma unroll
         for (int kt = 0; kt < 2; ++kt) {
             bhalf8 ah, al;
-            afrag_hl(h_hi, h_lo, srow + kt * 32 + g16 * 8, ah, al);
+            afrag32<false>(hp, kt * 32 + g16 * 8, ah, al);
             acc = mm3(ah, al, WH[2 + kt], WL[2 + kt], acc);
         }
+        const float* ap = s + (size_t)ar * 64;
 #pragma unroll
         for (int kt = 0; kt < 2; ++kt) {
             bhalf8 ah, al;
-            afrag_hl(s_hi, s_lo, (size_t)ar * 64 + kt * 32 + g16 * 8, ah, al);
+            afrag32<false>(ap, kt * 32 + g16 * 8, ah, al);
             acc = mm3(ah, al, WH[4 + kt], WL[4 + kt], acc);
         }
 #pragma unroll
         for (int i = 0; i < 4; ++i) {
             int r = rbase + ms * 16 + g16 * 4 + i;
-            if (r < N_NETS) {
-                float graw = acc[i] + bias;
-                if (g_raw) g_raw[(size_t)r * 64 + cs] = graw;
-                u16 hh, ll;
-                split1(leaky(graw), hh, ll);
-                g_hi[(size_t)r * 64 + cs] = hh;
-                g_lo[(size_t)r * 64 + cs] = ll;
-            }
+            if (r < N_NETS) g[(size_t)r * 64 + cs] = acc[i] + bias;
         }
     }
 }
 
 __global__ __launch_bounds__(256) void k_conv_node(
-    u16* h_hi, u16* h_lo, float* __restrict__ h_f32,
-    const u16* __restrict__ s_hi, const u16* __restrict__ s_lo,
+    float* __restrict__ h, const float* __restrict__ s,
     const u16* __restrict__ wfh, const u16* __restrict__ wfl, int wbase,
     const float* __restrict__ b)
 {
@@ -610,9 +518,10 @@
 #pragma unroll
     for (int ms = 0; ms < 4; ++ms) {
         int r = min(rbase + ms * 16 + l15, N_NODES - 1);
+        const float* rp = h + (size_t)r * 64;
 #pragma unroll
         for (int kt = 0; kt < 2; ++kt)
-            afrag_hl(h_hi, h_lo, (size_t)r * 64 + kt * 32 + g16 * 8, HH[ms][kt], HL[ms][kt]);
+            afrag32<false>(rp, kt * 32 + g16 * 8, HH[ms][kt], HL[ms][kt]);
     }
     __syncthreads();
 
@@ -623,23 +532,17 @@
 #pragma unroll
         for (int kt = 0; kt < 2; ++kt) acc = mm3(HH[ms][kt], HL[ms][kt], WH[kt], WL[kt], acc);
         int ar = min(rbase + ms * 16 + l15, N_NODES - 1);
+        const float* bp = s + (size_t)ar * 64;
 #pragma unroll
         for (int kt = 0; kt < 2; ++kt) {
             bhalf8 ah, al;
-            afrag_hl(s_hi, s_lo, (size_t)ar * 64 + kt * 32 + g16 * 8, ah, al);
+            afrag32<false>(bp, kt * 32 + g16 * 8, ah, al);
             acc = mm3(ah, al, WH[2 + kt], WL[2 + kt], acc);
         }
 #pragma unroll
         for (int i = 0; i < 4; ++i) {
             int r = rbase + ms * 16 + g16 * 4 + i;
-            if (r < N_NODES) {
-                float hval = leaky(acc[i] + bias);
-                if (h_f32) h_f32[(size_t)r * 64 + cs] = hval;
-                u16 hh, ll;
-                split1(hval, hh, ll);
-                h_hi[(size_t)r * 64 + cs] = hh;
-                h_lo[(size_t)r * 64 + cs] = ll;
-            }
+            if (r < N_NODES) h[(size_t)r * 64 + cs] = leaky(acc[i] + bias);
         }
     }
 }
@@ -666,7 +569,7 @@
 }
 
 __global__ __launch_bounds__(256) void k_fc_node(
-    float* __restrict__ out, const u16* __restrict__ h_hi, const u16* __restrict__ h_lo,
+    float* __restrict__ out, const float* __restrict__ h,
     const u16* __restrict__ wfh, const u16* __restrict__ wfl,
     const float* __restrict__ b1, const float* __restrict__ W2, const float* __restrict__ b2)
 {
@@ -696,7 +599,7 @@
         bhalf8 ah[2], al[2];
 #pragma unroll
         for (int kt = 0; kt < 2; ++kt)
-            afrag_hl(h_hi, h_lo, (size_t)r * 64 + kt * 32 + g16 * 8, ah[kt], al[kt]);
+            afrag32<false>(h + (size_t)r * 64, kt * 32 + g16 * 8, ah[kt], al[kt]);
         float po[4][4] = {{0.f,0.f,0.f,0.f},{0.f,0.f,0.f,0.f},{0.f,0.f,0.f,0.f},{0.f,0.f,0.f,0.f}};
 #pragma unroll
         for (int s = 0; s < 4; ++s) {
@@ -738,7 +641,7 @@
 }
 
 __global__ __launch_bounds__(256) void k_fc_net(
-    float* __restrict__ out, const u16* __restrict__ g_hi, const u16* __restrict__ g_lo,
+    float* __restrict__ out, const float* __restrict__ g,
     const u16* __restrict__ wfh, const u16* __restrict__ wfl,
     const float* __restrict__ b1, const float* __restrict__ W2, const float* __restrict__ b2)
 {
@@ -763,7 +666,7 @@
         bhalf8 ah[2], al[2];
 #pragma unroll
         for (int kt = 0; kt < 2; ++kt)
-            afrag_hl(g_hi, g_lo, (size_t)r * 64 + kt * 32 + g16 * 8, ah[kt], al[kt]);
+            afrag32<true>(g + (size_t)r * 64, kt * 32 + g16 * 8, ah[kt], al[kt]);
         floatx4 acc = {0.f, 0.f, 0.f, 0.f};
 #pragma unroll
         for (int kt = 0; kt < 2; ++kt) acc = mm3(ah[kt], al[kt], W1H[kt], W1L[kt], acc);
@@ -848,12 +751,9 @@
         used += (bytes + 255) & ~(size_t)255;
         return r;
     };
-    u16* h_hi = (u16*)alloc((size_t)N_NODES * 64 * 2);
-    u16* h_lo = (u16*)alloc((size_t)N_NODES * 64 * 2);
-    u16* g_hi = (u16*)alloc((size_t)N_NETS * 64 * 2);
-    u16* g_lo = (u16*)alloc((size_t)N_NETS * 64 * 2);
-    u16* s_hi = (u16*)alloc((size_t)N_NODES * 64 * 2);
-    u16* s_lo = (u16*)alloc((size_t)N_NODES * 64 * 2);
+    float* h  = (float*)alloc((size_t)N_NODES * 64 * 4);
+    float* g  = (float*)alloc((size_t)N_NETS * 64 * 4);
+    float* s  = (float*)alloc((size_t)N_NODES * 64 * 4);
     u16* wfh  = (u16*)alloc((size_t)W_TOTAL * 2);
     u16* wfl  = (u16*)alloc((size_t)W_TOTAL * 2);
     float* vn     = (float*)alloc((size_t)NUM_VN * EMB * 4);
@@ -874,18 +774,11 @@
     int* cnt_src  = cnt_node + N_NODES;
     int* cnt_vn   = cnt_src + N_NODES;
 
-    float* g_raw = nullptr;
-    if (used + (size_t)N_NETS * 64 * 4 + 256 <= ws_size)
-        g_raw = (float*)alloc((size_t)N_NETS * 64 * 4);
-    float* h_f32 = nullptr;
-    if (used + (size_t)N_NODES * 64 * 4 + 256 <= ws_size)
-        h_f32 = (float*)alloc((size_t)N_NODES * 64 * 4);
-
     const int nodeTiles = (N_NODES + 63) / 64;
     const int netTiles  = (N_NETS + 63) / 64;
     const int vnBlocks  = (NUM_VN + 3) / 4;
     const int vnElemBlocks  = (NUM_VN * EMB + 255) / 256;
-    const int addVnBlocks  = (N_NODES * 8 + 255) / 256;
+    const int addVnBlocks  = (N_NODES * 16 + 255) / 256;
     const int edgeThreadBlocks = (E_SINK + 255) / 256;
     const int miscThreadBlocks = (N_NODES + 255) / 256;
     const int netWaveBlocks  = (N_NETS + 3) / 4;
@@ -915,49 +808,30 @@
 
     k_prep_w<<<prepBlocks, 256, 0, stream>>>(ne_W1, ne_W2, te_W1, te_W2,
                                              conv_Wnet, conv_Wnode, fc1n_W, fc1e_W, wfh, wfl);
-    k_node_enc<<<nodeTiles, 256, 0, stream>>>(node_features, wfh, wfl, ne_b1, ne_b2,
-                                              h_hi, h_lo, h_f32);
-    k_net_enc<<<netTiles, 256, 0, stream>>>(net_features, wfh, wfl, te_b1, te_b2, g_hi, g_lo);
+    k_node_enc<<<nodeTiles, 256, 0, stream>>>(node_features, wfh, wfl, ne_b1, ne_b2, h);
+    k_net_enc<<<netTiles, 256, 0, stream>>>(net_features, wfh, wfl, te_b1, te_b2, g);
     k_vn_init<<<vnElemBlocks, 256, 0, stream>>>(vn, vn_emb);
 
     for (int l = 0; l < 3; ++l) {
-        k_add_vn<<<addVnBlocks, 256, 0, stream>>>(h_hi, h_lo, h_f32, vn, batch);
-
-        if (h_f32)
-            k_gather_agg<true><<<netWaveBlocks, 256, 0, stream>>>(s_hi, s_lo, h_hi, h_lo, h_f32,
-                                                                  net_start, e_pack);
-        else
-            k_gather_agg<false><<<netWaveBlocks, 256, 0, stream>>>(s_hi, s_lo, h_hi, h_lo, h_f32,
-                                                                   net_start, e_pack);
-
-        k_conv_net<<<netTiles, 256, 0, stream>>>(g_hi, g_lo, g_raw, h_hi, h_lo, s_hi, s_lo,
-            src_nodes, wfh, wfl, OFF_CWNET + l * 12288, conv_bnet + (size_t)l * 64);
-
-        if (g_raw)
-            k_gather_back<true><<<nodeWaveBlocks, 256, 0, stream>>>(s_hi, s_lo, g_hi, g_lo, g_raw,
-                src_start, s_net, node_start, e2_pack);
-        else
-            k_gather_back<false><<<nodeWaveBlocks, 256, 0, stream>>>(s_hi, s_lo, g_hi, g_lo, g_raw,
-                src_start, s_net, node_start, e2_pack);
-
-        k_conv_node<<<nodeTiles, 256, 0, stream>>>(h_hi, h_lo, h_f32, s_hi, s_lo,
+        k_add_vn<<<addVnBlocks, 256, 0, stream>>>((float4*)h, vn, batch);
+
+        k_gather_agg<<<netWaveBlocks, 256, 0, stream>>>(s, h, net_start, e_pack);
+        k_conv_net<<<netTiles, 256, 0, stream>>>(g, h, s, src_nodes,
+            wfh, wfl, OFF_CWNET + l * 12288, conv_bnet + (size_t)l * 64, l > 0 ? 1 : 0);
+
+        k_gather_back<<<nodeWaveBlocks, 256, 0, stream>>>(s, g,
+            src_start, s_net, node_start, e2_pack);
+        k_conv_node<<<nodeTiles, 256, 0, stream>>>(h, s,
             wfh, wfl, OFF_CWNODE + l * 8192, conv_bnode + (size_t)l * 64);
 
         if (l < 2) {
-            if (h_f32)
-                k_pool_gather<true><<<NUM_VN, 256, 0, stream>>>(pooled, h_hi, h_lo, h_f32,
-                                                                vn_start, b_node);
-            else
-                k_pool_gather<false><<<NUM_VN, 256, 0, stream>>>(pooled, h_hi, h_lo, h_f32,
-                                                                 vn_start, b_node);
+            k_pool_gather<<<NUM_VN, 256, 0, stream>>>(pooled, h, vn_start, b_node);
             k_vn_update<<<vnBlocks, 256, 0, stream>>>(vn, pooled,
                 vn_W1 + (size_t)l * 64 * 64, vn_b1 + (size_t)l * 64,
                 vn_W2 + (size_t)l * 64 * 64, vn_b2 + (size_t)l * 64);
         }
     }
 
-    k_fc_node<<<nodeTiles, 256, 0, stream>>>(out_node, h_hi, h_lo, wfh, wfl,
-                                             fc1n_b, fc2n_W, fc2n_b);
-    k_fc_net<<<netTiles, 256, 0, stream>>>(out_net, g_hi, g_lo, wfh, wfl,
-                                           fc1e_b, fc2e_W, fc2e_b);
-}
+    k_fc_node<<<nodeTiles, 256, 0, stream>>>(out_node, h, wfh, wfl, fc1n_b, fc2n_W, fc2n_b);
+    k_fc_net<<<netTiles, 256, 0, stream>>>(out_net, g, wfh, wfl, fc1e_b, fc2e_W, fc2e_b);
+}
```

Result: faster. 1.679 ms (-5.7%).
